# Kernel tuning notes

Measured on AMD Instinct MI355X. Metric: run time of the kernel, lower is better.

Reference implementation:

```python
import jax, jax.numpy as jnp
import numpy as np
from jax import lax

B, OBS, E, H = 65536, 20, 64, 64


def setup_inputs() -> dict:
    key = jax.random.key(0)
    ks = jax.random.split(key, 13)
    s = 0.1
    inp = {
        "obs_traj": jax.random.normal(ks[0], (B, OBS, 2), jnp.float32),
        "W_emb": jax.random.normal(ks[1], (E, 2), jnp.float32) * s,
        "b_emb": jax.random.normal(ks[2], (E,), jnp.float32) * s,
        "Wih_e": jax.random.normal(ks[3], (4 * H, E), jnp.float32) * s,
        "Whh_e": jax.random.normal(ks[4], (4 * H, H), jnp.float32) * s,
        "bih_e": jax.random.normal(ks[5], (4 * H,), jnp.float32) * s,
        "bhh_e": jax.random.normal(ks[6], (4 * H,), jnp.float32) * s,
        "Wih_d": jax.random.normal(ks[7], (4 * H, E), jnp.float32) * s,
        "Whh_d": jax.random.normal(ks[8], (4 * H, H), jnp.float32) * s,
        "bih_d": jax.random.normal(ks[9], (4 * H,), jnp.float32) * s,
        "bhh_d": jax.random.normal(ks[10], (4 * H,), jnp.float32) * s,
        "W_fc": jax.random.normal(ks[11], (2, H), jnp.float32) * s,
        "b_fc": jax.random.normal(ks[12], (2,), jnp.float32) * s,
        "pred_len": 12,
    }
    return inp


def _lstm_step(x, h, c, Wih, Whh, b):
    # PyTorch LSTM gate order: i, f, g, o
    g = x @ Wih.T + h @ Whh.T + b  # [B, 4H]
    i, f, gg, o = jnp.split(g, 4, axis=-1)
    c2 = jax.nn.sigmoid(f) * c + jax.nn.sigmoid(i) * jnp.tanh(gg)
    h2 = jax.nn.sigmoid(o) * jnp.tanh(c2)
    return h2, c2


def reference(obs_traj, W_emb, b_emb, Wih_e, Whh_e, bih_e, bhh_e,
              Wih_d, Whh_d, bih_d, bhh_d, W_fc, b_fc, pred_len):
    bsz = obs_traj.shape[0]
    dt = obs_traj.dtype
    # Encoder: embed all observed steps at once, then scan the LSTM over time.
    emb = jax.nn.relu(obs_traj @ W_emb.T + b_emb)  # [B, OBS, E]
    b_e = bih_e + bhh_e
    h0 = jnp.zeros((bsz, H), dt)
    c0 = jnp.zeros((bsz, H), dt)

    def enc_step(carry, x_t):
        h, c = carry
        h, c = _lstm_step(x_t, h, c, Wih_e, Whh_e, b_e)
        return (h, c), None

    (h, c), _ = lax.scan(enc_step, (h0, c0), jnp.swapaxes(emb, 0, 1))

    b_d = bih_d + bhh_d
    dec_in = jax.nn.relu(obs_traj[:, -1, :] @ W_emb.T + b_emb)  # [B, E]

    def dec_step(carry, _):
        h, c, x = carry
        h, c = _lstm_step(x, h, c, Wih_d, Whh_d, b_d)
        pred = h @ W_fc.T + b_fc  # [B, 2]
        nxt = jax.nn.relu(pred @ W_emb.T + b_emb)
        return (h, c, nxt), pred

    _, preds = lax.scan(dec_step, (h, c, dec_in), None, length=pred_len)
    return jnp.swapaxes(preds, 0, 1)  # [B, pred_len, 2]
```

## Files before the change

### kernel.cpp

```cpp
#include <hip/hip_runtime.h>

typedef __bf16 bf16x8 __attribute__((ext_vector_type(8)));
typedef __bf16 bf16x4 __attribute__((ext_vector_type(4)));
typedef float  f32x4  __attribute__((ext_vector_type(4)));
typedef float  f32x2  __attribute__((ext_vector_type(2)));

constexpr int BATCH = 65536;
constexpr int OBS   = 20;
constexpr int PRED  = 12;
constexpr int BT    = 64;
constexpr int AST   = 136;

constexpr float SIO = -1.4426950408889634f;
constexpr float SG  =  2.8853900817779268f;

__device__ __forceinline__ float exp2_(float x) { return __builtin_amdgcn_exp2f(x); }
__device__ __forceinline__ float rcp_(float x)  { return __builtin_amdgcn_rcpf(x); }

struct SmallW {
    float  biasf_e[256];
    float  biasf_d[256];
    float4 embc[64];
    float  wfc[128];
    float  bfc[2];
};

__global__ __launch_bounds__(256, 3)
void vanilla_lstm(const float* __restrict__ obs,
                  const float* __restrict__ W_emb, const float* __restrict__ b_emb,
                  const float* __restrict__ Wih_e, const float* __restrict__ Whh_e,
                  const float* __restrict__ bih_e, const float* __restrict__ bhh_e,
                  const float* __restrict__ Wih_d, const float* __restrict__ Whh_d,
                  const float* __restrict__ bih_d, const float* __restrict__ bhh_d,
                  const float* __restrict__ W_fc,  const float* __restrict__ b_fc,
                  float* __restrict__ out)
{
    __shared__ __align__(16) __bf16 As[BT * AST];
    __shared__ __align__(16) float  pred_s[BT * 2];
    __shared__ SmallW sw;

    const int tid  = threadIdx.x;
    const int wv   = tid >> 6;
    const int lane = tid & 63;
    const int m    = lane & 15;
    const int q    = lane >> 4;
    const int wblk = wv * 16;
    const size_t gRow0 = (size_t)blockIdx.x * BT;

    {
        const int wv_ = tid >> 6, c_ = (tid >> 4) & 3, qr = tid & 15;
        const int g = c_ * 64 + wv_ * 16 + qr;
        const float sc = (c_ == 2) ? SG : SIO;
        sw.biasf_e[tid] = sc * (bih_e[g] + bhh_e[g]);
        sw.biasf_d[tid] = sc * (bih_d[g] + bhh_d[g]);
    }
    if (tid < 64)  sw.embc[tid] = make_float4(W_emb[2 * tid], W_emb[2 * tid + 1], b_emb[tid], 0.f);
    if (tid < 128) sw.wfc[tid]  = W_fc[tid];
    if (tid < 2)   sw.bfc[tid]  = b_fc[tid];

    {
        uint4 z; z.x = z.y = z.z = z.w = 0u;
        uint4* p = (uint4*)As;
        constexpr int NV = BT * AST * 2 / 16;
        #pragma unroll
        for (int i = 0; i < NV / 256; ++i) p[tid + i * 256] = z;
        if (tid < (NV % 256)) p[tid + (NV / 256) * 256] = z;
    }

    bf16x8 bfr[4][4];
    auto load_bfr = [&](const float* Wih, const float* Whh) {
        #pragma unroll
        for (int c = 0; c < 4; ++c) {
            const float sc = (c == 2) ? SG : SIO;
            const int n = c * 64 + wblk + m;
            #pragma unroll
            for (int kt = 0; kt < 4; ++kt) {
                const float* s = (kt < 2) ? (Wih + n * 64 + kt * 32 + q * 8)
                                          : (Whh + n * 64 + (kt - 2) * 32 + q * 8);
                float4 a = *(const float4*)s;
                float4 b = *(const float4*)(s + 4);
                bf16x8 v;
                v[0] = (__bf16)(sc * a.x); v[1] = (__bf16)(sc * a.y);
                v[2] = (__bf16)(sc * a.z); v[3] = (__bf16)(sc * a.w);
                v[4] = (__bf16)(sc * b.x); v[5] = (__bf16)(sc * b.y);
                v[6] = (__bf16)(sc * b.z); v[7] = (__bf16)(sc * b.w);
                bfr[c][kt] = v;
            }
        }
    };
    load_bfr(Wih_e, Whh_e);

    f32x4 cst[4];
    #pragma unroll
    for (int i = 0; i < 4; ++i) cst[i] = f32x4{0.f, 0.f, 0.f, 0.f};

    __syncthreads();

    f32x4 acc[2][2][4];

    auto gemm = [&](int chunk, const float* bfrag) {
        #pragma unroll
        for (int c = 0; c < 4; ++c) {
            f32x4 b = *(const f32x4*)&bfrag[(wv * 4 + c) * 16 + q * 4];
            acc[chunk][0][c] = b;
            acc[chunk][1][c] = b;
        }
        #pragma unroll
        for (int kt = 0; kt < 4; ++kt) {
            bf16x8 af[2];
            #pragma unroll
            for (int sub = 0; sub < 2; ++sub)
                af[sub] = *(const bf16x8*)&As[(chunk * 32 + sub * 16 + m) * AST + kt * 32 + q * 8];
            #pragma unroll
            for (int sub = 0; sub < 2; ++sub)
                #pragma unroll
                for (int c = 0; c < 4; ++c)
                    acc[chunk][sub][c] = __builtin_amdgcn_mfma_f32_16x16x32_bf16(
                        bfr[c][kt], af[sub], acc[chunk][sub][c], 0, 0, 0);
        }
    };

    auto update = [&](int chunk) {
        #pragma unroll
        for (int sub = 0; sub < 2; ++sub) {
            const int idx = chunk * 2 + sub;
            const int row = chunk * 32 + sub * 16 + m;
            f32x4 ci = cst[idx];
            bf16x4 h4;
            #pragma unroll
            for (int r = 0; r < 4; ++r) {
                const float gi = acc[chunk][sub][0][r];
                const float gf = acc[chunk][sub][1][r];
                const float gg = acc[chunk][sub][2][r];
                const float go = acc[chunk][sub][3][r];
                const float Ef = exp2_(gf);
                const float a  = ci[r] * rcp_(1.0f + Ef);
                const float Ei = exp2_(gi);
                const float Eg = exp2_(gg);
                const float d1 = 1.0f + Ei;
                const float r1 = rcp_(fmaf(d1, Eg, d1));
                const float cN = fmaf(Eg - 1.0f, r1, a);
                const float Eo = exp2_(go);
                const float Ec = exp2_(cN * SG);
                const float d2 = 1.0f + Eo;
                const float r2 = rcp_(fmaf(d2, Ec, d2));
                const float h  = (Ec - 1.0f) * r2;
                ci[r] = cN;
                h4[r] = (__bf16)h;
            }
            cst[idx] = ci;
            *(bf16x4*)&As[row * AST + 64 + wblk + q * 4] = h4;
        }
    };

    auto emb_chunk = [&](int chunk, float o0, float o1) {
        const int row = chunk * 32 + (lane & 31);
        const int h8  = lane >> 5;
        bf16x8 v;
        #pragma unroll
        for (int j = 0; j < 8; ++j) {
            float4 wc = sw.embc[wblk + h8 * 8 + j];
            v[j] = (__bf16)fmaxf(fmaf(o0, wc.x, fmaf(o1, wc.y, wc.z)), 0.f);
        }
        *(bf16x8*)&As[row * AST + wblk + h8 * 8] = v;
    };

    const float* obr = obs + (gRow0 + (lane & 31)) * (OBS * 2);

    {
        f32x2 o0 = *(const f32x2*)obr;
        f32x2 o1 = *(const f32x2*)(obr + 32 * (OBS * 2));
        emb_chunk(0, o0[0], o0[1]);
        emb_chunk(1, o1[0], o1[1]);
    }
    __syncthreads();
    gemm(0, sw.biasf_e);

    for (int t = 0; t < OBS; ++t) {
        __syncthreads();
        f32x2 on0{0.f, 0.f};
        if (t + 1 < OBS) on0 = *(const f32x2*)(obr + (t + 1) * 2);
        update(0);
        gemm(1, sw.biasf_e);
        if (t + 1 < OBS) emb_chunk(0, on0[0], on0[1]);
        __syncthreads();
        f32x2 on1{0.f, 0.f};
        if (t + 1 < OBS) on1 = *(const f32x2*)(obr + 32 * (OBS * 2) + (t + 1) * 2);
        update(1);
        if (t + 1 < OBS) {
            gemm(0, sw.biasf_e);
            emb_chunk(1, on1[0], on1[1]);
        }
    }

    load_bfr(Wih_d, Whh_d);
    gemm(0, sw.biasf_d);

    auto pred_phase = [&](int chunk, int td) {
        const int row  = chunk * 32 + (tid >> 3);
        const int comp = (tid >> 2) & 1;
        const int seg  = tid & 3;
        bf16x8 h0 = *(const bf16x8*)&As[row * AST + 64 + seg * 16];
        bf16x8 h1 = *(const bf16x8*)&As[row * AST + 64 + seg * 16 + 8];
        f32x4 w0 = *(const f32x4*)&sw.wfc[comp * 64 + seg * 16];
        f32x4 w1 = *(const f32x4*)&sw.wfc[comp * 64 + seg * 16 + 4];
        f32x4 w2 = *(const f32x4*)&sw.wfc[comp * 64 + seg * 16 + 8];
        f32x4 w3 = *(const f32x4*)&sw.wfc[comp * 64 + seg * 16 + 12];
        float p = (float)h0[0] * w0[0] + (float)h0[1] * w0[1] + (float)h0[2] * w0[2] + (float)h0[3] * w0[3]
                + (float)h0[4] * w1[0] + (float)h0[5] * w1[1] + (float)h0[6] * w1[2] + (float)h0[7] * w1[3]
                + (float)h1[0] * w2[0] + (float)h1[1] * w2[1] + (float)h1[2] * w2[2] + (float)h1[3] * w2[3]
                + (float)h1[4] * w3[0] + (float)h1[5] * w3[1] + (float)h1[6] * w3[2] + (float)h1[7] * w3[3];
        p += __shfl_xor(p, 1, 64);
        p += __shfl_xor(p, 2, 64);
        if (seg == 0) {
            p += sw.bfc[comp];
            pred_s[row * 2 + comp] = p;
            out[((gRow0 + row) * PRED + td) * 2 + comp] = p;
        }
    };
    auto emb_dec = [&](int chunk) {
        const int row = chunk * 32 + (lane & 31);
        f32x2 pv = *(const f32x2*)&pred_s[row * 2];
        emb_chunk(chunk, pv[0], pv[1]);
    };

    for (int td = 0; td < PRED; ++td) {
        __syncthreads();
        update(0);
        gemm(1, sw.biasf_d);
        __syncthreads();
        update(1);
        pred_phase(0, td);
        __syncthreads();
        pred_phase(1, td);
        if (td + 1 < PRED) emb_dec(0);
        __syncthreads();
        if (td + 1 < PRED) {
            emb_dec(1);
            gemm(0, sw.biasf_d);
        }
    }
}

extern "C" void kernel_launch(void* const* d_in, const int* in_sizes, int n_in,
                              void* d_out, int out_size, void* d_ws, size_t ws_size,
                              hipStream_t stream) {
    (void)in_sizes; (void)n_in; (void)d_ws; (void)ws_size; (void)out_size;
    const float* obs   = (const float*)d_in[0];
    const float* W_emb = (const float*)d_in[1];
    const float* b_emb = (const float*)d_in[2];
    const float* Wih_e = (const float*)d_in[3];
    const float* Whh_e = (const float*)d_in[4];
    const float* bih_e = (const float*)d_in[5];
    const float* bhh_e = (const float*)d_in[6];
    const float* Wih_d = (const float*)d_in[7];
    const float* Whh_d = (const float*)d_in[8];
    const float* bih_d = (const float*)d_in[9];
    const float* bhh_d = (const float*)d_in[10];
    const float* W_fc  = (const float*)d_in[11];
    const float* b_fc  = (const float*)d_in[12];
    float* o = (float*)d_out;

    dim3 grid(BATCH / BT), block(256);
    hipLaunchKernelGGL(vanilla_lstm, grid, block, 0, stream,
                       obs, W_emb, b_emb, Wih_e, Whh_e, bih_e, bhh_e,
                       Wih_d, Whh_d, bih_d, bhh_d, W_fc, b_fc, o);
}
```

Before: 302.2 us.

## Move last Whh K-tile to LDS and share accumulators to fit four blocks per CU

One of the four K-tiles of recurrent weight fragments (the second half of Whh) now lives in shared memory instead of registers, filled per wave for the encoder and again for the decoder. The per-chunk accumulator array becomes a single shared set, since each update consumes it before the next gemm overwrites it. Together these cut VGPR usage enough to raise launch bounds from 3 to 4 blocks per CU, aiming to hide the latency of the serial recurrence with more resident waves. The cost is extra LDS reads in every gemm step and about 16 KB more LDS per block, which together must still fit four blocks per CU.

Result: slower. 314.7 us (+4.1%).

```diff
diff --git a/kernel.cpp b/kernel.cpp
--- a/kernel.cpp
+++ b/kernel.cpp
@@ -25,7 +25,7 @@
     float  bfc[2];
 };
 
-__global__ __launch_bounds__(256, 3)
+__global__ __launch_bounds__(256, 4)
 void vanilla_lstm(const float* __restrict__ obs,
                   const float* __restrict__ W_emb, const float* __restrict__ b_emb,
                   const float* __restrict__ Wih_e, const float* __restrict__ Whh_e,
@@ -36,6 +36,7 @@
                   float* __restrict__ out)
 {
     __shared__ __align__(16) __bf16 As[BT * AST];
+    __shared__ bf16x8 wkt3[1024];
     __shared__ __align__(16) float  pred_s[BT * 2];
     __shared__ SmallW sw;
 
@@ -67,16 +68,16 @@
         if (tid < (NV % 256)) p[tid + (NV / 256) * 256] = z;
     }
 
-    bf16x8 bfr[4][4];
+    bf16x8 bfr[4][3];
     auto load_bfr = [&](const float* Wih, const float* Whh) {
         #pragma unroll
         for (int c = 0; c < 4; ++c) {
             const float sc = (c == 2) ? SG : SIO;
             const int n = c * 64 + wblk + m;
             #pragma unroll
-            for (int kt = 0; kt < 4; ++kt) {
+            for (int kt = 0; kt < 3; ++kt) {
                 const float* s = (kt < 2) ? (Wih + n * 64 + kt * 32 + q * 8)
-                                          : (Whh + n * 64 + (kt - 2) * 32 + q * 8);
+                                          : (Whh + n * 64 + q * 8);
                 float4 a = *(const float4*)s;
                 float4 b = *(const float4*)(s + 4);
                 bf16x8 v;
@@ -88,7 +89,24 @@
             }
         }
     };
+    auto fill_wkt3 = [&](const float* Whh) {
+        #pragma unroll
+        for (int c = 0; c < 4; ++c) {
+            const float sc = (c == 2) ? SG : SIO;
+            const int n = c * 64 + wblk + m;
+            const float* s = Whh + n * 64 + 32 + q * 8;
+            float4 a = *(const float4*)s;
+            float4 b = *(const float4*)(s + 4);
+            bf16x8 v;
+            v[0] = (__bf16)(sc * a.x); v[1] = (__bf16)(sc * a.y);
+            v[2] = (__bf16)(sc * a.z); v[3] = (__bf16)(sc * a.w);
+            v[4] = (__bf16)(sc * b.x); v[5] = (__bf16)(sc * b.y);
+            v[6] = (__bf16)(sc * b.z); v[7] = (__bf16)(sc * b.w);
+            wkt3[(wv * 4 + c) * 64 + lane] = v;
+        }
+    };
     load_bfr(Wih_e, Whh_e);
+    fill_wkt3(Whh_e);
 
     f32x4 cst[4];
     #pragma unroll
@@ -96,27 +114,34 @@
 
     __syncthreads();
 
-    f32x4 acc[2][2][4];
+    f32x4 acc[2][4];
 
     auto gemm = [&](int chunk, const float* bfrag) {
         #pragma unroll
         for (int c = 0; c < 4; ++c) {
             f32x4 b = *(const f32x4*)&bfrag[(wv * 4 + c) * 16 + q * 4];
-            acc[chunk][0][c] = b;
-            acc[chunk][1][c] = b;
-        }
-        #pragma unroll
-        for (int kt = 0; kt < 4; ++kt) {
-            bf16x8 af[2];
-            #pragma unroll
-            for (int sub = 0; sub < 2; ++sub)
-                af[sub] = *(const bf16x8*)&As[(chunk * 32 + sub * 16 + m) * AST + kt * 32 + q * 8];
-            #pragma unroll
-            for (int sub = 0; sub < 2; ++sub)
-                #pragma unroll
-                for (int c = 0; c < 4; ++c)
-                    acc[chunk][sub][c] = __builtin_amdgcn_mfma_f32_16x16x32_bf16(
-                        bfr[c][kt], af[sub], acc[chunk][sub][c], 0, 0, 0);
+            acc[0][c] = b;
+            acc[1][c] = b;
+        }
+        #pragma unroll
+        for (int kt = 0; kt < 3; ++kt) {
+            bf16x8 af0 = *(const bf16x8*)&As[(chunk * 32 + m) * AST + kt * 32 + q * 8];
+            bf16x8 af1 = *(const bf16x8*)&As[(chunk * 32 + 16 + m) * AST + kt * 32 + q * 8];
+            #pragma unroll
+            for (int c = 0; c < 4; ++c) {
+                acc[0][c] = __builtin_amdgcn_mfma_f32_16x16x32_bf16(bfr[c][kt], af0, acc[0][c], 0, 0, 0);
+                acc[1][c] = __builtin_amdgcn_mfma_f32_16x16x32_bf16(bfr[c][kt], af1, acc[1][c], 0, 0, 0);
+            }
+        }
+        {
+            bf16x8 af0 = *(const bf16x8*)&As[(chunk * 32 + m) * AST + 96 + q * 8];
+            bf16x8 af1 = *(const bf16x8*)&As[(chunk * 32 + 16 + m) * AST + 96 + q * 8];
+            #pragma unroll
+            for (int c = 0; c < 4; ++c) {
+                bf16x8 w3 = wkt3[(wv * 4 + c) * 64 + lane];
+                acc[0][c] = __builtin_amdgcn_mfma_f32_16x16x32_bf16(w3, af0, acc[0][c], 0, 0, 0);
+                acc[1][c] = __builtin_amdgcn_mfma_f32_16x16x32_bf16(w3, af1, acc[1][c], 0, 0, 0);
+            }
         }
     };
 
@@ -129,10 +154,10 @@
             bf16x4 h4;
             #pragma unroll
             for (int r = 0; r < 4; ++r) {
-                const float gi = acc[chunk][sub][0][r];
-                const float gf = acc[chunk][sub][1][r];
-                const float gg = acc[chunk][sub][2][r];
-                const float go = acc[chunk][sub][3][r];
+                const float gi = acc[sub][0][r];
+                const float gf = acc[sub][1][r];
+                const float gg = acc[sub][2][r];
+                const float go = acc[sub][3][r];
                 const float Ef = exp2_(gf);
                 const float a  = ci[r] * rcp_(1.0f + Ef);
                 const float Ei = exp2_(gi);
@@ -194,6 +219,7 @@
     }
 
     load_bfr(Wih_d, Whh_d);
+    fill_wkt3(Whh_d);
     gemm(0, sw.biasf_d);
 
     auto pred_phase = [&](int chunk, int td) {
```
